# Kernel optimization log

Hardware: AMD Instinct MI355X
Metric: run time of the kernel (lower is better)

Reference implementation:

```python
import jax, jax.numpy as jnp
import numpy as np

H = 16   # num_heads
G = 4    # groups (code structurally requires 4)
DIM = 1024
HD = DIM // H // G  # 16


def setup_inputs() -> dict:
    key = jax.random.key(0)
    k1, k2, k3 = jax.random.split(key, 3)
    x = jax.random.normal(k1, (8, 4096, DIM), dtype=jnp.float32)
    w_qkvw = jax.random.normal(k2, (DIM, 4 * DIM), dtype=jnp.float32) * 0.02
    w_out = jax.random.normal(k3, (DIM, DIM), dtype=jnp.float32) * 0.02
    return {"x": x, "w_qkvw": w_qkvw, "w_out": w_out}


def reference(x, w_qkvw, w_out):
    B, S, dim = x.shape
    qkvw = x @ w_qkvw  # [B, S, 4*dim]
    # chunk into G groups along last dim -> G tensors of [B, S, dim] (G==4)
    chunks = jnp.split(qkvw, G, axis=-1)
    # each chunk split again into G sub-chunks of [B, S, dim/G]
    subs = [jnp.split(t, G, axis=-1) for t in chunks]
    # torch: q,k,v,w = [cat([qi,ki,vi,wi], dim=0) for qi,ki,vi,wi in zip(*subs)]
    q = jnp.concatenate([subs[i][0] for i in range(4)], axis=0)  # [4B, S, dim/G]
    k = jnp.concatenate([subs[i][1] for i in range(4)], axis=0)
    v = jnp.concatenate([subs[i][2] for i in range(4)], axis=0)
    w = jnp.concatenate([subs[i][3] for i in range(4)], axis=0)
    # faithful row-major reshape: [4B, S, dim/G] -> [4B, H, S, hd] -> transpose(1,2)
    def shp(t):
        return t.reshape(B * G, H, -1, HD).swapaxes(1, 2)  # [4B, S, H, hd]
    q, k, v = shp(q), shp(k), shp(v)
    w = w.reshape(B * G, H, -1, HD)  # [4B, H, S, hd]
    scale = HD ** -0.5
    scores = (q @ k.swapaxes(-2, -1)) * scale          # [4B, S, H, H]
    attn = jax.nn.softmax(scores, axis=-1)
    o = (attn @ v).swapaxes(1, 2).reshape(B, S, dim)   # [B, S, dim]
    return (o * w.reshape(B, S, dim)) @ w_out
```

## Files before the change

kernel.cpp:

```cpp
#include <hip/hip_runtime.h>
#include <hip/hip_bf16.h>
#include <stdint.h>


typedef __bf16 bf16;
typedef __bf16 bf16x8 __attribute__((ext_vector_type(8)));
typedef float f32x4 __attribute__((ext_vector_type(4)));

__device__ __forceinline__ void gload16(const bf16* g, bf16* l) {
  __builtin_amdgcn_global_load_lds(
      (const __attribute__((address_space(1))) void*)g,
      (__attribute__((address_space(3))) void*)l, 16, 0, 0);
}

#define BAR() asm volatile("s_barrier" ::: "memory")
#define SB() __builtin_amdgcn_sched_barrier(0)
#define LGKM0 asm volatile("s_waitcnt lgkmcnt(0)" ::: "memory")
#define PRIO1 __builtin_amdgcn_s_setprio(1)
#define PRIO0 __builtin_amdgcn_s_setprio(0)

#define READ_A(mq, AO)                                                        \
  {                                                                           \
    _Pragma("unroll") for (int i = 0; i < 4; ++i)                             \
        _Pragma("unroll") for (int kk = 0; kk < 2; ++kk)                      \
            a[i][kk] = *(const bf16x8*)(lds + (AO) +                          \
                                        ((mq)*64 + i * 16 + fr) * 128 +       \
                                        ((kk * 64 + fkb) ^ xo));              \
  }
#define READ_B(nh, BO)                                                        \
  {                                                                           \
    _Pragma("unroll") for (int j = 0; j < 2; ++j)                             \
        _Pragma("unroll") for (int kk = 0; kk < 2; ++kk)                      \
            b[(nh)*2 + j][kk] = *(const bf16x8*)(lds + (BO) +                 \
                                                 (bro + (nh)*32 + j * 16 + fr) * 128 + \
                                                 ((kk * 64 + fkb) ^ xo));     \
  }
#define MFMA_Q(mq, nh)                                                        \
  {                                                                           \
    _Pragma("unroll") for (int i = 0; i < 4; ++i)                             \
        _Pragma("unroll") for (int j = 0; j < 2; ++j) {                       \
      acc[(mq)*4 + i][(nh)*2 + j] = __builtin_amdgcn_mfma_f32_16x16x32_bf16(  \
          a[i][0], b[(nh)*2 + j][0], acc[(mq)*4 + i][(nh)*2 + j], 0, 0, 0);   \
      acc[(mq)*4 + i][(nh)*2 + j] = __builtin_amdgcn_mfma_f32_16x16x32_bf16(  \
          a[i][1], b[(nh)*2 + j][1], acc[(mq)*4 + i][(nh)*2 + j], 0, 0, 0);   \
    }                                                                         \
  }
#define STAGE_A(h, X)                                                         \
  {                                                                           \
    const int ro = ((X)&1) * 65536 + (h)*16384;                               \
    const bf16* g = gA + ((h)*128) * 1024 + (X)*64;                           \
    gload16(g, (bf16*)(lds + ro + wv * 1024));                                \
    gload16(g + 64 * 1024, (bf16*)(lds + ro + 8192 + wv * 1024));             \
  }
#define STAGE_B(h, X)                                                         \
  {                                                                           \
    const int ro = ((X)&1) * 65536 + 32768 + (h)*16384;                       \
    const bf16* g = gB + ((h)*128) * 1024 + (X)*64;                           \
    gload16(g, (bf16*)(lds + ro + wv * 1024));                                \
    gload16(g + 64 * 1024, (bf16*)(lds + ro + 8192 + wv * 1024));             \
  }

template <typename OutT>
__global__ __launch_bounds__(512, 2)
void gemm256(const bf16* __restrict__ A, const bf16* __restrict__ BT,
             OutT* __restrict__ C, int N) {
  constexpr int K = 1024;
  __shared__ __align__(16) char smem[131072];
  char* lds = smem;

  const int tid = threadIdx.x;
  const int lane = tid & 63;
  const int wv = tid >> 6;
  const int wr = wv >> 2;
  const int wc = wv & 3;

  const int gx = gridDim.x;
  const int nwg = gx * gridDim.y;
  const int bid = blockIdx.y * gx + blockIdx.x;
  const int swz = (bid & 7) * (nwg >> 3) + (bid >> 3);
  const long row0 = (long)(swz / gx) * 256;
  const long col0 = (long)(swz % gx) * 256;

  const int srow = tid >> 3;
  const int scol = (((tid & 7) * 16) ^ ((srow & 7) << 4)) >> 1;
  const bf16* gA = A + (row0 + srow) * K + scol;
  const bf16* gB = BT + (col0 + srow) * K + scol;

  const int fr = lane & 15;
  const int fkb = (lane >> 4) * 16;
  const int xo = (fr & 7) << 4;
  const int bro = (wc & 1) * 64;

  bf16x8 a[4][2], b[4][2];
  f32x4 acc[8][4] = {};

  STAGE_A(0, 0); STAGE_A(1, 0); STAGE_B(0, 0); STAGE_B(1, 0);
  STAGE_B(0, 1); STAGE_B(1, 1);
  asm volatile("s_waitcnt vmcnt(4)" ::: "memory");
  SB(); BAR(); SB();
  {
    const int aoff0 = wr * 16384;
    const int boff0 = 32768 + (wc >> 1) * 16384;
    READ_A(0, aoff0); READ_B(0, boff0);
  }
  SB();

  for (int T = 0; T < 16; ++T) {
    const int d = T & 1;
    const int aoff = d * 65536 + wr * 16384;
    const int boff = d * 65536 + 32768 + (wc >> 1) * 16384;
    const int aoffN = (d ^ 1) * 65536 + wr * 16384;
    const int boffN = (d ^ 1) * 65536 + 32768 + (wc >> 1) * 16384;
    if (T < 15) { STAGE_A(0, T + 1); STAGE_A(1, T + 1); }
    SB(); BAR(); LGKM0; SB();
    READ_B(1, boff); SB();
    PRIO1; MFMA_Q(0, 0); PRIO0; SB();
    BAR(); LGKM0; SB();
    PRIO1; MFMA_Q(0, 1); PRIO0; SB();
    READ_A(1, aoff); SB();
    BAR(); LGKM0; SB();
    PRIO1; MFMA_Q(1, 1); PRIO0; SB();
    if (T < 14) {
      STAGE_B(0, T + 2); STAGE_B(1, T + 2);
      asm volatile("s_waitcnt vmcnt(4)" ::: "memory");
    } else if (T == 14) {
      asm volatile("s_waitcnt vmcnt(0)" ::: "memory");
    }
    SB(); BAR(); LGKM0; SB();
    PRIO1; MFMA_Q(1, 0); PRIO0; SB();
    if (T < 15) { READ_A(0, aoffN); READ_B(0, boffN); }
    SB();
  }

  const int crow = (lane >> 4) * 4;
  const int ccol = lane & 15;
  const long rb = row0 + wr * 128;
  const long cb = col0 + wc * 64;
#pragma unroll
  for (int m = 0; m < 8; ++m)
#pragma unroll
    for (int n = 0; n < 4; ++n)
#pragma unroll
      for (int i = 0; i < 4; ++i)
        C[(rb + m * 16 + crow + i) * (long)N + cb + n * 16 + ccol] =
            (OutT)acc[m][n][i];
}

__device__ __forceinline__ void load16f(const bf16* p, float* f) {
  const uint4* u = (const uint4*)p;
  uint4 a = u[0], b = u[1];
  uint32_t w[8] = {a.x, a.y, a.z, a.w, b.x, b.y, b.z, b.w};
#pragma unroll
  for (int j = 0; j < 8; ++j) {
    f[2 * j] = __uint_as_float(w[j] << 16);
    f[2 * j + 1] = __uint_as_float(w[j] & 0xffff0000u);
  }
}

__global__ __launch_bounds__(256)
void attn_fuse(const bf16* __restrict__ qkvw, bf16* __restrict__ ow,
               int b0, long bstride) {
  __shared__ bf16 data[16 * 1024];
  const int s_hi = blockIdx.x;
  const int g = blockIdx.y;
  const int bz = blockIdx.z;
  const int b = b0 + bz;
  const bf16* base = qkvw + (long)bz * bstride;
  const int tid = threadIdx.x;

#pragma unroll
  for (int i = 0; i < 8; ++i) {
    int c = tid + i * 256;
    int h = c >> 7;
    int col = (c & 127) * 8;
    *(uint4*)&data[h * 1024 + col] =
        *(const uint4*)(base + (long)(h * 256 + s_hi) * 4096 + g * 1024 + col);
  }
  __syncthreads();

  const int s_lo = tid >> 4;
  const int h1 = tid & 15;
  const int off = s_lo * 16;

  float q[16], p[16], o[16];
  load16f(&data[h1 * 1024 + off], q);

  float mx = -1e30f;
#pragma unroll
  for (int h2 = 0; h2 < 16; ++h2) {
    float kf[16];
    load16f(&data[h2 * 1024 + 256 + off], kf);
    float s = 0.f;
#pragma unroll
    for (int d = 0; d < 16; ++d) s += q[d] * kf[d];
    s *= 0.25f;
    p[h2] = s;
    mx = fmaxf(mx, s);
  }
  float sum = 0.f;
#pragma unroll
  for (int h2 = 0; h2 < 16; ++h2) {
    float e = __expf(p[h2] - mx);
    p[h2] = e;
    sum += e;
  }
  const float inv = 1.f / sum;
#pragma unroll
  for (int d = 0; d < 16; ++d) o[d] = 0.f;
#pragma unroll
  for (int h2 = 0; h2 < 16; ++h2) {
    float vf[16];
    load16f(&data[h2 * 1024 + 512 + off], vf);
    const float av = p[h2] * inv;
#pragma unroll
    for (int d = 0; d < 16; ++d) o[d] += av * vf[d];
  }
  float wf[16];
  load16f(&data[h1 * 1024 + 768 + off], wf);

  const int bp = g * 8 + b;
  const long R = (long)(bp >> 2) * 4096 + (bp & 3) * 1024 + h1 * 64 + (s_hi >> 2);
  const int cbo = (s_hi & 3) * 256 + off;
  union { uint4 u[2]; bf16 hh[16]; } st;
#pragma unroll
  for (int d = 0; d < 16; ++d) st.hh[d] = (bf16)(o[d] * wf[d]);
  uint4* dst = (uint4*)&ow[R * 1024 + cbo];
  dst[0] = st.u[0];
  dst[1] = st.u[1];
}

__global__ __launch_bounds__(256)
void cast_x_kernel(const float* __restrict__ in, bf16* __restrict__ out, long n4) {
  long i = (long)blockIdx.x * 256 + threadIdx.x;
  if (i >= n4) return;
  float4 v = ((const float4*)in)[i];
  union { uint2 d; bf16 h[4]; } r;
  r.h[0] = (bf16)v.x; r.h[1] = (bf16)v.y; r.h[2] = (bf16)v.z; r.h[3] = (bf16)v.w;
  ((uint2*)out)[i] = r.d;
}

__global__ __launch_bounds__(256)
void tcast_kernel(const float* __restrict__ in, bf16* __restrict__ out, int R, int C) {
  __shared__ float t[64][65];
  const int c0 = blockIdx.x * 64, r0 = blockIdx.y * 64;
  const int lr = threadIdx.x >> 6;
  const int lc = threadIdx.x & 63;
#pragma unroll
  for (int i = 0; i < 16; ++i)
    t[lr + i * 4][lc] = in[(long)(r0 + lr + i * 4) * C + c0 + lc];
  __syncthreads();
#pragma unroll
  for (int i = 0; i < 16; ++i) {
    int oc = lr + i * 4;
    out[(long)(c0 + oc) * R + r0 + lc] = (bf16)t[lc][oc];
  }
}

extern "C" void kernel_launch(void* const* d_in, const int* in_sizes, int n_in,
                              void* d_out, int out_size, void* d_ws, size_t ws_size,
                              hipStream_t stream) {
  const float* x = (const float*)d_in[0];
  const float* w_qkvw = (const float*)d_in[1];
  const float* w_out = (const float*)d_in[2];
  float* out = (float*)d_out;

  char* ws = (char*)d_ws;
  size_t off = 0;
  bf16* x_bf = (bf16*)(ws + off); off += (size_t)32768 * 1024 * 2;
  bf16* bt1  = (bf16*)(ws + off); off += (size_t)4096 * 1024 * 2;
  bf16* bt2  = (bf16*)(ws + off); off += (size_t)1024 * 1024 * 2;
  bf16* owb  = (bf16*)(ws + off); off += (size_t)32768 * 1024 * 2;
  bf16* qk   = (bf16*)(ws + off);
  const size_t rem = ws_size > off ? ws_size - off : 0;
  const size_t full_need = (size_t)32768 * 4096 * 2;

  cast_x_kernel<<<32768, 256, 0, stream>>>(x, x_bf, (long)8388608);
  tcast_kernel<<<dim3(64, 16), 256, 0, stream>>>(w_qkvw, bt1, 1024, 4096);
  tcast_kernel<<<dim3(16, 16), 256, 0, stream>>>(w_out, bt2, 1024, 1024);

  if (rem >= full_need) {
    gemm256<bf16><<<dim3(16, 128), 512, 0, stream>>>(x_bf, bt1, qk, 4096);
    attn_fuse<<<dim3(256, 4, 8), 256, 0, stream>>>(qk, owb, 0, (long)4096 * 4096);
  } else {
    for (int b = 0; b < 8; ++b) {
      gemm256<bf16><<<dim3(16, 16), 512, 0, stream>>>(
          x_bf + (size_t)b * 4096 * 1024, bt1, qk, 4096);
      attn_fuse<<<dim3(256, 4, 1), 256, 0, stream>>>(qk, owb, b, 0);
    }
  }
  gemm256<float><<<dim3(4, 128), 512, 0, stream>>>(owb, bt2, out, 1024);
}
```

Baseline: 463.2 us.

## Triple-buffer A tiles in LDS and add supertile block swizzle for GEMMs

The GEMM kernel moves from double-buffering both operands in one 128 KB LDS region to triple-buffering the A tile with rotating offsets, keeping B double-buffered, in 160 KB of LDS. A-tile prefetch now runs two K-steps ahead, and the vmcnt wait is raised to match. It also adds an optional supertile mapping from block to tile, grouping 8x4 tiles per XCD to improve L2 reuse of A and B. The larger LDS footprint leaves no headroom for a second block per CU, and the deeper prefetch raises the number of outstanding loads.

```diff
diff --git a/kernel.cpp b/kernel.cpp
--- a/kernel.cpp
+++ b/kernel.cpp
@@ -45,16 +45,15 @@
           a[i][1], b[(nh)*2 + j][1], acc[(mq)*4 + i][(nh)*2 + j], 0, 0, 0);   \
     }                                                                         \
   }
-#define STAGE_A(h, X)                                                         \
-  {                                                                           \
-    const int ro = ((X)&1) * 65536 + (h)*16384;                               \
+#define STAGE_AH(h, X, base)                                                  \
+  {                                                                           \
     const bf16* g = gA + ((h)*128) * 1024 + (X)*64;                           \
-    gload16(g, (bf16*)(lds + ro + wv * 1024));                                \
-    gload16(g + 64 * 1024, (bf16*)(lds + ro + 8192 + wv * 1024));             \
-  }
-#define STAGE_B(h, X)                                                         \
-  {                                                                           \
-    const int ro = ((X)&1) * 65536 + 32768 + (h)*16384;                       \
+    gload16(g, (bf16*)(lds + (base) + (h)*16384 + wv * 1024));                \
+    gload16(g + 64 * 1024, (bf16*)(lds + (base) + (h)*16384 + 8192 + wv * 1024)); \
+  }
+#define STAGE_BH(h, X)                                                        \
+  {                                                                           \
+    const int ro = 98304 + ((X)&1) * 32768 + (h)*16384;                       \
     const bf16* g = gB + ((h)*128) * 1024 + (X)*64;                           \
     gload16(g, (bf16*)(lds + ro + wv * 1024));                                \
     gload16(g + 64 * 1024, (bf16*)(lds + ro + 8192 + wv * 1024));             \
@@ -63,9 +62,9 @@
 template <typename OutT>
 __global__ __launch_bounds__(512, 2)
 void gemm256(const bf16* __restrict__ A, const bf16* __restrict__ BT,
-             OutT* __restrict__ C, int N) {
+             OutT* __restrict__ C, int N, int super) {
   constexpr int K = 1024;
-  __shared__ __align__(16) char smem[131072];
+  __shared__ __align__(16) char smem[163840];
   char* lds = smem;
 
   const int tid = threadIdx.x;
@@ -77,9 +76,21 @@
   const int gx = gridDim.x;
   const int nwg = gx * gridDim.y;
   const int bid = blockIdx.y * gx + blockIdx.x;
-  const int swz = (bid & 7) * (nwg >> 3) + (bid >> 3);
-  const long row0 = (long)(swz / gx) * 256;
-  const long col0 = (long)(swz % gx) * 256;
+  const int xcd = bid & 7;
+  const int l = bid >> 3;
+  long trow, tcol;
+  if (super) {
+    const int s = l >> 5, i = l & 31;
+    const int colS = gx >> 2;
+    trow = xcd * 16 + (s / colS) * 8 + (i >> 2);
+    tcol = (s % colS) * 4 + (i & 3);
+  } else {
+    const int swz = xcd * (nwg >> 3) + l;
+    trow = swz / gx;
+    tcol = swz % gx;
+  }
+  const long row0 = trow * 256;
+  const long col0 = tcol * 256;
 
   const int srow = tid >> 3;
   const int scol = (((tid & 7) * 16) ^ ((srow & 7) << 4)) >> 1;
@@ -94,24 +105,23 @@
   bf16x8 a[4][2], b[4][2];
   f32x4 acc[8][4] = {};
 
-  STAGE_A(0, 0); STAGE_A(1, 0); STAGE_B(0, 0); STAGE_B(1, 0);
-  STAGE_B(0, 1); STAGE_B(1, 1);
+  STAGE_AH(0, 0, 0); STAGE_AH(1, 0, 0);
+  STAGE_AH(0, 1, 32768); STAGE_AH(1, 1, 32768);
+  STAGE_BH(0, 0); STAGE_BH(1, 0);
+  STAGE_BH(0, 1); STAGE_BH(1, 1);
   asm volatile("s_waitcnt vmcnt(4)" ::: "memory");
   SB(); BAR(); SB();
-  {
-    const int aoff0 = wr * 16384;
-    const int boff0 = 32768 + (wc >> 1) * 16384;
-    READ_A(0, aoff0); READ_B(0, boff0);
-  }
+  READ_A(0, wr * 16384);
+  READ_B(0, 98304 + (wc >> 1) * 16384);
   SB();
 
+  int ac0 = 0, ac1 = 32768, ac2 = 65536;
   for (int T = 0; T < 16; ++T) {
-    const int d = T & 1;
-    const int aoff = d * 65536 + wr * 16384;
-    const int boff = d * 65536 + 32768 + (wc >> 1) * 16384;
-    const int aoffN = (d ^ 1) * 65536 + wr * 16384;
-    const int boffN = (d ^ 1) * 65536 + 32768 + (wc >> 1) * 16384;
-    if (T < 15) { STAGE_A(0, T + 1); STAGE_A(1, T + 1); }
+    const int aoff = ac0 + wr * 16384;
+    const int aoffN = ac1 + wr * 16384;
+    const int boff = 98304 + (T & 1) * 32768 + (wc >> 1) * 16384;
+    const int boffN = 98304 + ((T + 1) & 1) * 32768 + (wc >> 1) * 16384;
+    if (T < 14) { STAGE_AH(0, T + 2, ac2); STAGE_AH(1, T + 2, ac2); }
     SB(); BAR(); LGKM0; SB();
     READ_B(1, boff); SB();
     PRIO1; MFMA_Q(0, 0); PRIO0; SB();
@@ -121,8 +131,8 @@
     BAR(); LGKM0; SB();
     PRIO1; MFMA_Q(1, 1); PRIO0; SB();
     if (T < 14) {
-      STAGE_B(0, T + 2); STAGE_B(1, T + 2);
-      asm volatile("s_waitcnt vmcnt(4)" ::: "memory");
+      STAGE_BH(0, T + 2); STAGE_BH(1, T + 2);
+      asm volatile("s_waitcnt vmcnt(8)" ::: "memory");
     } else if (T == 14) {
       asm volatile("s_waitcnt vmcnt(0)" ::: "memory");
     }
@@ -130,6 +140,7 @@
     PRIO1; MFMA_Q(1, 0); PRIO0; SB();
     if (T < 15) { READ_A(0, aoffN); READ_B(0, boffN); }
     SB();
+    const int t = ac0; ac0 = ac1; ac1 = ac2; ac2 = t;
   }
 
   const int crow = (lane >> 4) * 4;
@@ -279,14 +290,14 @@
   tcast_kernel<<<dim3(16, 16), 256, 0, stream>>>(w_out, bt2, 1024, 1024);
 
   if (rem >= full_need) {
-    gemm256<bf16><<<dim3(16, 128), 512, 0, stream>>>(x_bf, bt1, qk, 4096);
+    gemm256<bf16><<<dim3(16, 128), 512, 0, stream>>>(x_bf, bt1, qk, 4096, 1);
     attn_fuse<<<dim3(256, 4, 8), 256, 0, stream>>>(qk, owb, 0, (long)4096 * 4096);
   } else {
     for (int b = 0; b < 8; ++b) {
       gemm256<bf16><<<dim3(16, 16), 512, 0, stream>>>(
-          x_bf + (size_t)b * 4096 * 1024, bt1, qk, 4096);
+          x_bf + (size_t)b * 4096 * 1024, bt1, qk, 4096, 0);
       attn_fuse<<<dim3(256, 4, 1), 256, 0, stream>>>(qk, owb, b, 0);
     }
   }
-  gemm256<float><<<dim3(4, 128), 512, 0, stream>>>(owb, bt2, out, 1024);
-}
+  gemm256<float><<<dim3(4, 128), 512, 0, stream>>>(owb, bt2, out, 1024, 1);
+}
```

Measured after the change: 458.3 us. About the same (-1.1%).
